# Kernel optimization log

Measured on AMD Instinct MI355X. Metric: run time of the kernel, lower is better.

## Reference

```python
import jax, jax.numpy as jnp
import numpy as np

N_PTS = 100000
C_IN, C_OUT, K = 16, 32, 3
B, D, H, W = 2, 32, 128, 128


def setup_inputs() -> dict:
    key = jax.random.key(0)
    kf, kw, kb, kz, ky, kx = jax.random.split(key, 6)
    features = jax.random.normal(kf, (N_PTS, C_IN), dtype=jnp.float32)
    coords = jnp.stack([
        jax.random.randint(kb, (N_PTS,), 0, B),
        jax.random.randint(kz, (N_PTS,), 0, D),
        jax.random.randint(ky, (N_PTS,), 0, H),
        jax.random.randint(kx, (N_PTS,), 0, W),
    ], axis=1).astype(jnp.int32)
    weight = jax.random.normal(kw, (K ** 3, C_IN, C_OUT), dtype=jnp.float32) * 0.01
    bias = jnp.zeros((C_OUT,), dtype=jnp.float32)
    return {"features": features, "coords": coords, "weight": weight, "bias": bias,
            "batch_size": B, "d_sp": D, "h_sp": H, "w_sp": W}


def reference(features, coords, weight, bias, batch_size, d_sp, h_sp, w_sp):
    # Scatter sparse voxel features into dense grid (B, C_in, D, H, W).
    n, c_in = features.shape
    c_out = weight.shape[2]
    k = K
    b, z, y, x = coords[:, 0], coords[:, 1], coords[:, 2], coords[:, 3]
    dense = jnp.zeros((batch_size, c_in, d_sp, h_sp, w_sp), dtype=features.dtype)
    dense = dense.at[b, :, z, y, x].set(features)  # (N,) advanced idx -> rows of (N, C_in)
    # Conv3d: torch copies weight.view(C_out, C_in, k, k, k) -> OIDHW kernel.
    kernel = weight.reshape(c_out, c_in, k, k, k)
    out = jax.lax.conv_general_dilated(
        dense, kernel,
        window_strides=(1, 1, 1),
        padding=[(1, 1), (1, 1), (1, 1)],
        dimension_numbers=("NCDHW", "OIDHW", "NCDHW"))
    out = jax.nn.relu(out + bias[None, :, None, None, None])
    # Dense equivalent of the torch nonzero-gather (which has data-dependent
    # shape): return the full dense activated grid (B, C_out, D, H, W).
    return out
```

## Files before the change

kernel.cpp:

```cpp
#include <hip/hip_runtime.h>

#define CIN   16
#define COUT  32
#define BATCH 2
#define DSP   32
#define HSP   128
#define WSP   128

#define TZ 4
#define TY 8
#define TX 16
#define NTZ 8
#define NTY 16
#define NTX 8
#define NTILES (BATCH*NTZ*NTY*NTX)
#define PZ 6
#define PY 10
#define PX 18
#define PVOX (PZ*PY*PX)
#define HALFU (PVOX*8)
#define BIN_CAP 128
#define NPAIR 14
#define NWREP ((NPAIR*2*64*8 + 255)/256)
#define NZB   ((NTILES + 255)/256)

typedef __bf16 bf16x8 __attribute__((ext_vector_type(8)));
typedef float  f32x4  __attribute__((ext_vector_type(4)));

__global__ void k_prep(const int4* __restrict__ coords, int n, int nbDedup,
                       int* __restrict__ map,
                       const float* __restrict__ w, __bf16* __restrict__ wpack,
                       int* __restrict__ binCnt) {
    int bb = blockIdx.x;
    if (bb < nbDedup) {
        int p = bb * 256 + threadIdx.x;
        if (p >= n) return;
        int4 c = coords[p];
        int vox = ((c.x*DSP + c.y)*HSP + c.z)*WSP + c.w;
        atomicMax(&map[vox], p);
    } else if (bb < nbDedup + NWREP) {
        int i = (bb - nbDedup) * 256 + threadIdx.x;
        if (i >= NPAIR*2*64*8) return;
        int j = i & 7, l = (i>>3) & 63, h = (i>>9) & 1, p = i >> 10;
        int tap = 2*p + ((l>>4)>>1);
        int co  = h*16 + (l & 15);
        int ci  = ((l>>4)&1)*8 + j;
        float v = (tap < 27) ? w[(co*CIN + ci)*27 + tap] : 0.0f;
        wpack[i] = (__bf16)v;
    } else {
        int i = (bb - nbDedup - NWREP) * 256 + threadIdx.x;
        if (i < NTILES) binCnt[i] = 0;
    }
}

__global__ void k_bin(const int4* __restrict__ coords, const int* __restrict__ map,
                      int* __restrict__ binCnt, int2* __restrict__ bins, int n) {
    int p = blockIdx.x * 256 + threadIdx.x;
    if (p >= n) return;
    int4 c = coords[p];
    int vox = ((c.x*DSP + c.y)*HSP + c.z)*WSP + c.w;
    if (map[vox] != p) return;
    int tile = ((c.x*NTZ + (c.y>>2))*NTY + (c.z>>3))*NTX + (c.w>>4);
    int slot = atomicAdd(&binCnt[tile], 1);
    if (slot < BIN_CAP)
        bins[tile*BIN_CAP + slot] = make_int2(p, (c.y<<14) | (c.z<<7) | c.w);
}

__global__ __launch_bounds__(256, 4) void k_conv(
    const float* __restrict__ feat, const __bf16* __restrict__ wpack,
    const float* __restrict__ bias, const int* __restrict__ binCnt,
    const int2* __restrict__ bins, float* __restrict__ out)
{
    __shared__ __align__(16) ushort patch[2*HALFU];
    __shared__ int ldsNt[27], ldsCnt[27], ldsPre[27];

    int tile = blockIdx.x;
    int txi = tile & 7;
    int tyi = (tile >> 3) & 15;
    int tzi = (tile >> 7) & 7;
    int b   = tile >> 10;
    int z0 = tzi*TZ, y0 = tyi*TY, x0 = txi*TX;

    int tid  = threadIdx.x;
    int lane = tid & 63, wave = tid >> 6;

    if (tid < 27) {
        int dz = tid/9 - 1, dy = (tid/3)%3 - 1, dx = tid%3 - 1;
        int nz = tzi+dz, ny = tyi+dy, nx = txi+dx;
        bool ok = (unsigned)nz < NTZ && (unsigned)ny < NTY && (unsigned)nx < NTX;
        int nt = ((b*NTZ + nz)*NTY + ny)*NTX + nx;
        ldsNt[tid]  = ok ? nt : 0;
        int c = ok ? binCnt[nt] : 0;
        ldsCnt[tid] = c > BIN_CAP ? BIN_CAP : c;
    }

    uint4* p4 = (uint4*)patch;
    for (int i = tid; i < 2*HALFU/8; i += 256) p4[i] = make_uint4(0,0,0,0);

    int lx16  = lane & 15;
    int lhalf = (lane >> 4) & 1;
    int ltp   = (lane >> 4) >> 1;

    int voff[NPAIR];
    #pragma unroll
    for (int p = 0; p < NPAIR; ++p) {
        int tap = 2*p + ltp; if (tap > 26) tap = 26;
        int kd = tap/9, kh = (tap/3)%3, kw = tap%3;
        voff[p] = (kd*PY + kh)*PX + kw;
    }

    float bv0 = bias[lx16], bv1 = bias[16 + lx16];

    __syncthreads();

    if (tid < 32) {
        int c = (tid < 27) ? ldsCnt[tid] : 0;
        #pragma unroll
        for (int off = 1; off < 32; off <<= 1) {
            int nvl = __shfl_up(c, off);
            if (tid >= off) c += nvl;
        }
        if (tid < 27) ldsPre[tid] = c;
    }
    __syncthreads();

    int total = ldsPre[26];
    #pragma unroll 2
    for (int i = tid; i < total; i += 256) {
        int lo = 0, hi = 26;
        #pragma unroll
        for (int it = 0; it < 5; ++it) {
            int mid = (lo + hi) >> 1;
            if (i < ldsPre[mid]) hi = mid; else lo = mid + 1;
        }
        int k = lo;
        int idx = i - (k ? ldsPre[k-1] : 0);
        int2 e = bins[ldsNt[k]*BIN_CAP + idx];
        int pz = e.y >> 14, py = (e.y >> 7) & 127, px = e.y & 127;
        int lz = pz - z0 + 1, ly = py - y0 + 1, lx = px - x0 + 1;
        if ((unsigned)lz < PZ && (unsigned)ly < PY && (unsigned)lx < PX) {
            const float4* fp = (const float4*)(feat + (size_t)e.x*CIN);
            float4 f0 = fp[0], f1 = fp[1], f2 = fp[2], f3 = fp[3];
            bf16x8 vlo = { (__bf16)f0.x,(__bf16)f0.y,(__bf16)f0.z,(__bf16)f0.w,
                           (__bf16)f1.x,(__bf16)f1.y,(__bf16)f1.z,(__bf16)f1.w };
            bf16x8 vhi = { (__bf16)f2.x,(__bf16)f2.y,(__bf16)f2.z,(__bf16)f2.w,
                           (__bf16)f3.x,(__bf16)f3.y,(__bf16)f3.z,(__bf16)f3.w };
            int v = (lz*PY + ly)*PX + lx;
            *(bf16x8*)(patch + v*8)         = vlo;
            *(bf16x8*)(patch + HALFU + v*8) = vhi;
        }
    }
    __syncthreads();

    const ushort* pb = patch + lhalf*HALFU + ((wave*PY)*PX + lx16)*8;
    f32x4 acc[8][2];
    #pragma unroll
    for (int gi = 0; gi < 8; ++gi) {
        acc[gi][0] = (f32x4){0.f,0.f,0.f,0.f};
        acc[gi][1] = (f32x4){0.f,0.f,0.f,0.f};
    }
    bf16x8 w0 = *(const bf16x8*)(wpack + (size_t)(0*64 + lane)*8);
    bf16x8 w1 = *(const bf16x8*)(wpack + (size_t)(1*64 + lane)*8);
    #pragma unroll
    for (int p = 0; p < NPAIR; ++p) {
        int pn = (p + 1 < NPAIR) ? p + 1 : 0;
        bf16x8 nw0 = *(const bf16x8*)(wpack + (size_t)((pn*2+0)*64 + lane)*8);
        bf16x8 nw1 = *(const bf16x8*)(wpack + (size_t)((pn*2+1)*64 + lane)*8);
        const ushort* pa = pb + voff[p]*8;
        #pragma unroll
        for (int gi = 0; gi < 8; ++gi) {
            bf16x8 a = *(const bf16x8*)(pa + gi*(PX*8));
            acc[gi][0] = __builtin_amdgcn_mfma_f32_16x16x32_bf16(a, w0, acc[gi][0], 0,0,0);
            acc[gi][1] = __builtin_amdgcn_mfma_f32_16x16x32_bf16(a, w1, acc[gi][1], 0,0,0);
        }
        w0 = nw0; w1 = nw1;
    }

    #pragma unroll
    for (int gi = 0; gi < 8; ++gi) {
        int gz = z0 + wave, gy = y0 + gi, gx = x0 + ((lane >> 4) << 2);
        f32x4 o0, o1;
        o0[0] = fmaxf(acc[gi][0][0]+bv0, 0.f); o0[1] = fmaxf(acc[gi][0][1]+bv0, 0.f);
        o0[2] = fmaxf(acc[gi][0][2]+bv0, 0.f); o0[3] = fmaxf(acc[gi][0][3]+bv0, 0.f);
        o1[0] = fmaxf(acc[gi][1][0]+bv1, 0.f); o1[1] = fmaxf(acc[gi][1][1]+bv1, 0.f);
        o1[2] = fmaxf(acc[gi][1][2]+bv1, 0.f); o1[3] = fmaxf(acc[gi][1][3]+bv1, 0.f);
        size_t base0 = ((((size_t)b*COUT + lx16)*DSP + gz)*HSP + gy)*WSP + gx;
        size_t base1 = base0 + (size_t)16*DSP*HSP*WSP;
        __builtin_nontemporal_store(o0, (f32x4*)(out + base0));
        __builtin_nontemporal_store(o1, (f32x4*)(out + base1));
    }
}

extern "C" void kernel_launch(void* const* d_in, const int* in_sizes, int n_in,
                              void* d_out, int out_size, void* d_ws, size_t ws_size,
                              hipStream_t stream) {
    const float* feat   = (const float*)d_in[0];
    const int4*  coords = (const int4*)d_in[1];
    const float* weight = (const float*)d_in[2];
    const float* bias   = (const float*)d_in[3];
    float* out = (float*)d_out;
    int n = in_sizes[0] / CIN;

    int*    map    = (int*)d_ws;
    int*    binCnt = map + BATCH*DSP*HSP*WSP;
    int2*   bins   = (int2*)(binCnt + NTILES);
    __bf16* wpack  = (__bf16*)(bins + NTILES*BIN_CAP);

    hipMemsetAsync(map, 0xFF, (size_t)BATCH*DSP*HSP*WSP*sizeof(int), stream);

    int nb = (n + 255) / 256;
    k_prep<<<nb + NWREP + NZB, 256, 0, stream>>>(coords, n, nb, map, weight, wpack, binCnt);
    k_bin <<<nb, 256, 0, stream>>>(coords, map, binCnt, bins, n);
    k_conv<<<NTILES, 256, 0, stream>>>(feat, wpack, bias, binCnt, bins, out);
}
```

Baseline: 75.34 us.

## Replace tile binning with a dense bf16 grid scatter and reshape conv tiles

```diff
diff --git a/kernel.cpp b/kernel.cpp
--- a/kernel.cpp
+++ b/kernel.cpp
@@ -6,31 +6,29 @@
 #define DSP   32
 #define HSP   128
 #define WSP   128
+#define NVOX  (BATCH*DSP*HSP*WSP)
 
 #define TZ 4
-#define TY 8
-#define TX 16
+#define TY 4
+#define TX 32
 #define NTZ 8
-#define NTY 16
-#define NTX 8
+#define NTY 32
+#define NTX 4
 #define NTILES (BATCH*NTZ*NTY*NTX)
 #define PZ 6
-#define PY 10
-#define PX 18
-#define PVOX (PZ*PY*PX)
+#define PYY 6
+#define PXX 34
+#define PVOX (PZ*PYY*PXX)
 #define HALFU (PVOX*8)
-#define BIN_CAP 128
 #define NPAIR 14
 #define NWREP ((NPAIR*2*64*8 + 255)/256)
-#define NZB   ((NTILES + 255)/256)
 
 typedef __bf16 bf16x8 __attribute__((ext_vector_type(8)));
 typedef float  f32x4  __attribute__((ext_vector_type(4)));
 
 __global__ void k_prep(const int4* __restrict__ coords, int n, int nbDedup,
                        int* __restrict__ map,
-                       const float* __restrict__ w, __bf16* __restrict__ wpack,
-                       int* __restrict__ binCnt) {
+                       const float* __restrict__ w, __bf16* __restrict__ wpack) {
     int bb = blockIdx.x;
     if (bb < nbDedup) {
         int p = bb * 256 + threadIdx.x;
@@ -38,7 +36,7 @@
         int4 c = coords[p];
         int vox = ((c.x*DSP + c.y)*HSP + c.z)*WSP + c.w;
         atomicMax(&map[vox], p);
-    } else if (bb < nbDedup + NWREP) {
+    } else {
         int i = (bb - nbDedup) * 256 + threadIdx.x;
         if (i >= NPAIR*2*64*8) return;
         int j = i & 7, l = (i>>3) & 63, h = (i>>9) & 1, p = i >> 10;
@@ -47,56 +45,43 @@
         int ci  = ((l>>4)&1)*8 + j;
         float v = (tap < 27) ? w[(co*CIN + ci)*27 + tap] : 0.0f;
         wpack[i] = (__bf16)v;
-    } else {
-        int i = (bb - nbDedup - NWREP) * 256 + threadIdx.x;
-        if (i < NTILES) binCnt[i] = 0;
     }
 }
 
-__global__ void k_bin(const int4* __restrict__ coords, const int* __restrict__ map,
-                      int* __restrict__ binCnt, int2* __restrict__ bins, int n) {
+__global__ void k_scatter(const int4* __restrict__ coords, const int* __restrict__ map,
+                          const float* __restrict__ feat, __bf16* __restrict__ dense,
+                          int n) {
     int p = blockIdx.x * 256 + threadIdx.x;
     if (p >= n) return;
     int4 c = coords[p];
     int vox = ((c.x*DSP + c.y)*HSP + c.z)*WSP + c.w;
     if (map[vox] != p) return;
-    int tile = ((c.x*NTZ + (c.y>>2))*NTY + (c.z>>3))*NTX + (c.w>>4);
-    int slot = atomicAdd(&binCnt[tile], 1);
-    if (slot < BIN_CAP)
-        bins[tile*BIN_CAP + slot] = make_int2(p, (c.y<<14) | (c.z<<7) | c.w);
+    const float4* fp = (const float4*)(feat + (size_t)p*CIN);
+    float4 f0 = fp[0], f1 = fp[1], f2 = fp[2], f3 = fp[3];
+    bf16x8 lo = { (__bf16)f0.x,(__bf16)f0.y,(__bf16)f0.z,(__bf16)f0.w,
+                  (__bf16)f1.x,(__bf16)f1.y,(__bf16)f1.z,(__bf16)f1.w };
+    bf16x8 hi = { (__bf16)f2.x,(__bf16)f2.y,(__bf16)f2.z,(__bf16)f2.w,
+                  (__bf16)f3.x,(__bf16)f3.y,(__bf16)f3.z,(__bf16)f3.w };
+    __bf16* d = dense + (size_t)vox*CIN;
+    *(bf16x8*)d       = lo;
+    *(bf16x8*)(d + 8) = hi;
 }
 
 __global__ __launch_bounds__(256, 4) void k_conv(
-    const float* __restrict__ feat, const __bf16* __restrict__ wpack,
-    const float* __restrict__ bias, const int* __restrict__ binCnt,
-    const int2* __restrict__ bins, float* __restrict__ out)
+    const __bf16* __restrict__ dense, const __bf16* __restrict__ wpack,
+    const float* __restrict__ bias, float* __restrict__ out)
 {
     __shared__ __align__(16) ushort patch[2*HALFU];
-    __shared__ int ldsNt[27], ldsCnt[27], ldsPre[27];
 
     int tile = blockIdx.x;
-    int txi = tile & 7;
-    int tyi = (tile >> 3) & 15;
+    int txi = tile & 3;
+    int tyi = (tile >> 2) & 31;
     int tzi = (tile >> 7) & 7;
     int b   = tile >> 10;
     int z0 = tzi*TZ, y0 = tyi*TY, x0 = txi*TX;
 
     int tid  = threadIdx.x;
     int lane = tid & 63, wave = tid >> 6;
-
-    if (tid < 27) {
-        int dz = tid/9 - 1, dy = (tid/3)%3 - 1, dx = tid%3 - 1;
-        int nz = tzi+dz, ny = tyi+dy, nx = txi+dx;
-        bool ok = (unsigned)nz < NTZ && (unsigned)ny < NTY && (unsigned)nx < NTX;
-        int nt = ((b*NTZ + nz)*NTY + ny)*NTX + nx;
-        ldsNt[tid]  = ok ? nt : 0;
-        int c = ok ? binCnt[nt] : 0;
-        ldsCnt[tid] = c > BIN_CAP ? BIN_CAP : c;
-    }
-
-    uint4* p4 = (uint4*)patch;
-    for (int i = tid; i < 2*HALFU/8; i += 256) p4[i] = make_uint4(0,0,0,0);
-
     int lx16  = lane & 15;
     int lhalf = (lane >> 4) & 1;
     int ltp   = (lane >> 4) >> 1;
@@ -106,59 +91,33 @@
     for (int p = 0; p < NPAIR; ++p) {
         int tap = 2*p + ltp; if (tap > 26) tap = 26;
         int kd = tap/9, kh = (tap/3)%3, kw = tap%3;
-        voff[p] = (kd*PY + kh)*PX + kw;
+        voff[p] = (kd*PYY + kh)*PXX + kw;
     }
-
     float bv0 = bias[lx16], bv1 = bias[16 + lx16];
 
-    __syncthreads();
-
-    if (tid < 32) {
-        int c = (tid < 27) ? ldsCnt[tid] : 0;
-        #pragma unroll
-        for (int off = 1; off < 32; off <<= 1) {
-            int nvl = __shfl_up(c, off);
-            if (tid >= off) c += nvl;
+    for (int u = tid; u < 2*PVOX; u += 256) {
+        int v  = u >> 1, h = u & 1;
+        int pz = v / (PYY*PXX);
+        int rem = v - pz*(PYY*PXX);
+        int py = rem / PXX;
+        int px = rem - py*PXX;
+        int gz = z0 - 1 + pz, gy = y0 - 1 + py, gx = x0 - 1 + px;
+        uint4 val = make_uint4(0,0,0,0);
+        if ((unsigned)gz < DSP && (unsigned)gy < HSP && (unsigned)gx < WSP) {
+            size_t vox = (((size_t)b*DSP + gz)*HSP + gy)*WSP + gx;
+            val = ((const uint4*)(dense + vox*CIN))[h];
         }
-        if (tid < 27) ldsPre[tid] = c;
+        *(uint4*)(patch + h*HALFU + v*8) = val;
     }
     __syncthreads();
 
-    int total = ldsPre[26];
-    #pragma unroll 2
-    for (int i = tid; i < total; i += 256) {
-        int lo = 0, hi = 26;
-        #pragma unroll
-        for (int it = 0; it < 5; ++it) {
-            int mid = (lo + hi) >> 1;
-            if (i < ldsPre[mid]) hi = mid; else lo = mid + 1;
-        }
-        int k = lo;
-        int idx = i - (k ? ldsPre[k-1] : 0);
-        int2 e = bins[ldsNt[k]*BIN_CAP + idx];
-        int pz = e.y >> 14, py = (e.y >> 7) & 127, px = e.y & 127;
-        int lz = pz - z0 + 1, ly = py - y0 + 1, lx = px - x0 + 1;
-        if ((unsigned)lz < PZ && (unsigned)ly < PY && (unsigned)lx < PX) {
-            const float4* fp = (const float4*)(feat + (size_t)e.x*CIN);
-            float4 f0 = fp[0], f1 = fp[1], f2 = fp[2], f3 = fp[3];
-            bf16x8 vlo = { (__bf16)f0.x,(__bf16)f0.y,(__bf16)f0.z,(__bf16)f0.w,
-                           (__bf16)f1.x,(__bf16)f1.y,(__bf16)f1.z,(__bf16)f1.w };
-            bf16x8 vhi = { (__bf16)f2.x,(__bf16)f2.y,(__bf16)f2.z,(__bf16)f2.w,
-                           (__bf16)f3.x,(__bf16)f3.y,(__bf16)f3.z,(__bf16)f3.w };
-            int v = (lz*PY + ly)*PX + lx;
-            *(bf16x8*)(patch + v*8)         = vlo;
-            *(bf16x8*)(patch + HALFU + v*8) = vhi;
-        }
-    }
-    __syncthreads();
-
-    const ushort* pb = patch + lhalf*HALFU + ((wave*PY)*PX + lx16)*8;
     f32x4 acc[8][2];
     #pragma unroll
     for (int gi = 0; gi < 8; ++gi) {
         acc[gi][0] = (f32x4){0.f,0.f,0.f,0.f};
         acc[gi][1] = (f32x4){0.f,0.f,0.f,0.f};
     }
+    const ushort* pb = patch + lhalf*HALFU + ((wave*PYY)*PXX + lx16)*8;
     bf16x8 w0 = *(const bf16x8*)(wpack + (size_t)(0*64 + lane)*8);
     bf16x8 w1 = *(const bf16x8*)(wpack + (size_t)(1*64 + lane)*8);
     #pragma unroll
@@ -169,7 +128,8 @@
         const ushort* pa = pb + voff[p]*8;
         #pragma unroll
         for (int gi = 0; gi < 8; ++gi) {
-            bf16x8 a = *(const bf16x8*)(pa + gi*(PX*8));
+            int y = gi >> 1, xg = gi & 1;
+            bf16x8 a = *(const bf16x8*)(pa + (y*PXX + xg*16)*8);
             acc[gi][0] = __builtin_amdgcn_mfma_f32_16x16x32_bf16(a, w0, acc[gi][0], 0,0,0);
             acc[gi][1] = __builtin_amdgcn_mfma_f32_16x16x32_bf16(a, w1, acc[gi][1], 0,0,0);
         }
@@ -178,7 +138,8 @@
 
     #pragma unroll
     for (int gi = 0; gi < 8; ++gi) {
-        int gz = z0 + wave, gy = y0 + gi, gx = x0 + ((lane >> 4) << 2);
+        int y = gi >> 1, xg = gi & 1;
+        int gz = z0 + wave, gy = y0 + y, gx = x0 + xg*16 + ((lane >> 4) << 2);
         f32x4 o0, o1;
         o0[0] = fmaxf(acc[gi][0][0]+bv0, 0.f); o0[1] = fmaxf(acc[gi][0][1]+bv0, 0.f);
         o0[2] = fmaxf(acc[gi][0][2]+bv0, 0.f); o0[3] = fmaxf(acc[gi][0][3]+bv0, 0.f);
@@ -201,15 +162,15 @@
     float* out = (float*)d_out;
     int n = in_sizes[0] / CIN;
 
-    int*    map    = (int*)d_ws;
-    int*    binCnt = map + BATCH*DSP*HSP*WSP;
-    int2*   bins   = (int2*)(binCnt + NTILES);
-    __bf16* wpack  = (__bf16*)(bins + NTILES*BIN_CAP);
+    int*    map   = (int*)d_ws;
+    __bf16* dense = (__bf16*)(map + NVOX);
+    __bf16* wpack = dense + (size_t)NVOX*CIN;
 
-    hipMemsetAsync(map, 0xFF, (size_t)BATCH*DSP*HSP*WSP*sizeof(int), stream);
+    hipMemsetAsync(map, 0xFF, (size_t)NVOX*sizeof(int), stream);
+    hipMemsetAsync(dense, 0, (size_t)NVOX*CIN*sizeof(__bf16), stream);
 
     int nb = (n + 255) / 256;
-    k_prep<<<nb + NWREP + NZB, 256, 0, stream>>>(coords, n, nb, map, weight, wpack, binCnt);
-    k_bin <<<nb, 256, 0, stream>>>(coords, map, binCnt, bins, n);
-    k_conv<<<NTILES, 256, 0, stream>>>(feat, wpack, bias, binCnt, bins, out);
+    k_prep   <<<nb + NWREP, 256, 0, stream>>>(coords, n, nb, map, weight, wpack);
+    k_scatter<<<nb, 256, 0, stream>>>(coords, map, feat, dense, n);
+    k_conv   <<<NTILES, 256, 0, stream>>>(dense, wpack, bias, out);
 }
```

Result: slower. 80.74 us (+7.2%).
